# Performance work log

Hardware: AMD Instinct MI355X
Metric: run time of the kernel (lower is better)

The kernel has to match this reference:

```python
import jax, jax.numpy as jnp
import numpy as np

EMBED_DIM = 1024
NUM_HEADS = 16
DEPTH = EMBED_DIM // NUM_HEADS


def setup_inputs() -> dict:
    key = jax.random.key(0)
    ks = jax.random.split(key, 6)
    B, S, D = 2, 2048, EMBED_DIM
    scale = 1.0 / np.sqrt(D)
    return {
        "x": jax.random.normal(ks[0], (B, S, D), dtype=jnp.float32),
        "mask": jax.random.randint(ks[1], (B, S), 0, 2, dtype=jnp.int32),
        "wq_w": jax.random.normal(ks[2], (D, D), dtype=jnp.float32) * scale,
        "wq_b": jnp.zeros((D,), dtype=jnp.float32),
        "wk_w": jax.random.normal(ks[3], (D, D), dtype=jnp.float32) * scale,
        "wk_b": jnp.zeros((D,), dtype=jnp.float32),
        "wv_w": jax.random.normal(ks[4], (D, D), dtype=jnp.float32) * scale,
        "wv_b": jnp.zeros((D,), dtype=jnp.float32),
        "dense_w": jax.random.normal(ks[5], (D, D), dtype=jnp.float32) * scale,
        "dense_b": jnp.zeros((D,), dtype=jnp.float32),
    }


def _split_heads(t, B, S):
    # [B, S, D] -> [B, H, S, depth]
    return t.reshape(B, S, NUM_HEADS, DEPTH).transpose(0, 2, 1, 3)


def reference(x, mask, wq_w, wq_b, wk_w, wk_b, wv_w, wv_b, dense_w, dense_b):
    B, S, D = x.shape
    q = _split_heads(x @ wq_w.T + wq_b, B, S)  # [B, H, S, d]
    k = _split_heads(x @ wk_w.T + wk_b, B, S)
    v = _split_heads(x @ wv_w.T + wv_b, B, S)

    logits = jnp.einsum('bhqd,bhkd->bhqk', q, k) / jnp.sqrt(
        jnp.asarray(DEPTH, dtype=jnp.float32))
    # mask [B, S] broadcast to [B, 1, 1, S] over key axis, additive -1e9
    logits = logits + mask.astype(logits.dtype)[:, None, None, :] * (-1e9)
    attn = jax.nn.softmax(logits, axis=-1)  # [B, H, S, S]
    ctx = jnp.einsum('bhqk,bhkd->bhqd', attn, v)
    ctx = ctx.transpose(0, 2, 1, 3).reshape(B, S, D)
    out = ctx @ dense_w.T + dense_b
    return out, attn
```

## Files before the change

### kernel.cpp

```cpp
#include <hip/hip_runtime.h>


#define S_LEN 2048
#define D_DIM 1024
#define H_NUM 16
#define M_ROWS 4096

typedef __attribute__((ext_vector_type(8))) short bf16x8;
typedef __attribute__((ext_vector_type(4))) float f32x4;

static __device__ __forceinline__ unsigned short f2bf(float f) {
  union { float f; unsigned u; } v; v.f = f;
  unsigned r = (v.u + 0x7FFFu + ((v.u >> 16) & 1u)) >> 16;
  return (unsigned short)r;
}

static __device__ __forceinline__ bf16x8 cvt8(float4 a, float4 b) {
  bf16x8 r;
  r[0] = (short)f2bf(a.x); r[1] = (short)f2bf(a.y);
  r[2] = (short)f2bf(a.z); r[3] = (short)f2bf(a.w);
  r[4] = (short)f2bf(b.x); r[5] = (short)f2bf(b.y);
  r[6] = (short)f2bf(b.z); r[7] = (short)f2bf(b.w);
  return r;
}

template <int AF32, int CF32>
__global__ __launch_bounds__(256) void gemm_bt(
    const void* __restrict__ Ap,
    const float* __restrict__ W0, const float* __restrict__ W1,
    const float* __restrict__ W2,
    const float* __restrict__ b0, const float* __restrict__ b1,
    const float* __restrict__ b2,
    void* __restrict__ C0v, void* __restrict__ C1v, void* __restrict__ C2v,
    int Mdim, int Ndim, int Kdim) {
  const float* W = W0; const float* bias = b0; void* Cv = C0v;
  if (blockIdx.z == 1) { W = W1; bias = b1; Cv = C1v; }
  else if (blockIdx.z == 2) { W = W2; bias = b2; Cv = C2v; }

  __shared__ __align__(16) unsigned short As[128][40];
  __shared__ __align__(16) unsigned short Bs[128][40];

  const int tid = threadIdx.x;
  const int l = tid & 63;
  const int w = tid >> 6;
  const int wm = w >> 1, wn = w & 1;
  const int lo = l & 15, hi = l >> 4;

  const int mBase = blockIdx.y * 128;
  const int nBase = blockIdx.x * 128;

  f32x4 acc[4][4];
  for (int mr = 0; mr < 4; ++mr)
    for (int nr = 0; nr < 4; ++nr) acc[mr][nr] = (f32x4){0.f, 0.f, 0.f, 0.f};

  for (int k0 = 0; k0 < Kdim; k0 += 32) {
    __syncthreads();
    for (int it = 0; it < 2; ++it) {
      int c = tid + it * 256;
      int r = c >> 2, cc = (c & 3) * 8;
      if (AF32) {
        const float* ap = (const float*)Ap + (size_t)(mBase + r) * Kdim + k0 + cc;
        *(bf16x8*)&As[r][cc] = cvt8(((const float4*)ap)[0], ((const float4*)ap)[1]);
      } else {
        *(int4*)&As[r][cc] =
            *(const int4*)((const unsigned short*)Ap + (size_t)(mBase + r) * Kdim + k0 + cc);
      }
      const float* wp = W + (size_t)(nBase + r) * Kdim + k0 + cc;
      *(bf16x8*)&Bs[r][cc] = cvt8(((const float4*)wp)[0], ((const float4*)wp)[1]);
    }
    __syncthreads();
    bf16x8 af[4], bfm[4];
    for (int mr = 0; mr < 4; ++mr)
      af[mr] = *(const bf16x8*)&As[wm * 64 + mr * 16 + lo][hi * 8];
    for (int nr = 0; nr < 4; ++nr)
      bfm[nr] = *(const bf16x8*)&Bs[wn * 64 + nr * 16 + lo][hi * 8];
    for (int mr = 0; mr < 4; ++mr)
      for (int nr = 0; nr < 4; ++nr)
        acc[mr][nr] = __builtin_amdgcn_mfma_f32_16x16x32_bf16(
            af[mr], bfm[nr], acc[mr][nr], 0, 0, 0);
  }

  for (int nr = 0; nr < 4; ++nr) {
    int col = nBase + wn * 64 + nr * 16 + lo;
    float bv = bias[col];
    for (int mr = 0; mr < 4; ++mr) {
      int rbase = mBase + wm * 64 + mr * 16 + hi * 4;
      for (int i = 0; i < 4; ++i) {
        float val = acc[mr][nr][i] + bv;
        if (CF32)
          ((float*)Cv)[(size_t)(rbase + i) * Ndim + col] = val;
        else
          ((unsigned short*)Cv)[(size_t)(rbase + i) * Ndim + col] = f2bf(val);
      }
    }
  }
}

__global__ __launch_bounds__(256) void attn_kernel(
    const unsigned short* __restrict__ qb, const unsigned short* __restrict__ kb,
    const unsigned short* __restrict__ vb, const int* __restrict__ mask,
    float* __restrict__ attn, unsigned short* __restrict__ ctx) {
  const int b = blockIdx.z, h = blockIdx.y, q0 = blockIdx.x * 64;
  const int tid = threadIdx.x, l = tid & 63, w = tid >> 6;
  const int lo = l & 15, hi = l >> 4;

  __shared__ __align__(16) unsigned short k_lds[64][72];
  __shared__ __align__(16) unsigned short vt_lds[64][72];
  __shared__ __align__(16) float p_f32[64][68];

  const size_t qrow = (size_t)(b * S_LEN + q0 + w * 16 + lo) * D_DIM + h * 64;
  bf16x8 qa[2];
  qa[0] = *(const bf16x8*)(qb + qrow + hi * 8);
  qa[1] = *(const bf16x8*)(qb + qrow + 32 + hi * 8);

  const size_t kvbase = (size_t)b * S_LEN * D_DIM + h * 64;
  float rsum[4] = {0.f, 0.f, 0.f, 0.f};

  for (int kt = 0; kt < 32; ++kt) {
    const int key0 = kt * 64;
    __syncthreads();
    for (int it = 0; it < 2; ++it) {
      int c = tid + it * 256;
      int r = c >> 3, cc = (c & 7) * 8;
      *(int4*)&k_lds[r][cc] = *(const int4*)(kb + kvbase + (size_t)(key0 + r) * D_DIM + cc);
    }
    __syncthreads();
    f32x4 acc[4];
    for (int nr = 0; nr < 4; ++nr) acc[nr] = (f32x4){0.f, 0.f, 0.f, 0.f};
    for (int nr = 0; nr < 4; ++nr) {
      bf16x8 kf0 = *(const bf16x8*)&k_lds[nr * 16 + lo][hi * 8];
      bf16x8 kf1 = *(const bf16x8*)&k_lds[nr * 16 + lo][32 + hi * 8];
      acc[nr] = __builtin_amdgcn_mfma_f32_16x16x32_bf16(qa[0], kf0, acc[nr], 0, 0, 0);
      acc[nr] = __builtin_amdgcn_mfma_f32_16x16x32_bf16(qa[1], kf1, acc[nr], 0, 0, 0);
    }
    for (int nr = 0; nr < 4; ++nr) {
      float madd = mask[b * S_LEN + key0 + nr * 16 + lo] ? -1e9f : 0.f;
      for (int i = 0; i < 4; ++i)
        rsum[i] += __expf(acc[nr][i] * 0.125f + madd);
    }
  }
  for (int m = 1; m < 16; m <<= 1)
    for (int i = 0; i < 4; ++i) rsum[i] += __shfl_xor(rsum[i], m);
  float inv[4];
  for (int i = 0; i < 4; ++i) inv[i] = 1.0f / rsum[i];

  f32x4 ctxacc[4];
  for (int nr = 0; nr < 4; ++nr) ctxacc[nr] = (f32x4){0.f, 0.f, 0.f, 0.f};
  const size_t attnbase = (size_t)(b * H_NUM + h) * S_LEN * S_LEN;

  for (int kt = 0; kt < 32; ++kt) {
    const int key0 = kt * 64;
    __syncthreads();
    for (int it = 0; it < 2; ++it) {
      int c = tid + it * 256;
      int r = c >> 3, cc = (c & 7) * 8;
      *(int4*)&k_lds[r][cc] = *(const int4*)(kb + kvbase + (size_t)(key0 + r) * D_DIM + cc);
      bf16x8 vv = *(const bf16x8*)(vb + kvbase + (size_t)(key0 + r) * D_DIM + cc);
      for (int j = 0; j < 8; ++j) vt_lds[cc + j][r] = (unsigned short)vv[j];
    }
    __syncthreads();
    f32x4 acc[4];
    for (int nr = 0; nr < 4; ++nr) acc[nr] = (f32x4){0.f, 0.f, 0.f, 0.f};
    for (int nr = 0; nr < 4; ++nr) {
      bf16x8 kf0 = *(const bf16x8*)&k_lds[nr * 16 + lo][hi * 8];
      bf16x8 kf1 = *(const bf16x8*)&k_lds[nr * 16 + lo][32 + hi * 8];
      acc[nr] = __builtin_amdgcn_mfma_f32_16x16x32_bf16(qa[0], kf0, acc[nr], 0, 0, 0);
      acc[nr] = __builtin_amdgcn_mfma_f32_16x16x32_bf16(qa[1], kf1, acc[nr], 0, 0, 0);
    }
    for (int nr = 0; nr < 4; ++nr) {
      float madd = mask[b * S_LEN + key0 + nr * 16 + lo] ? -1e9f : 0.f;
      for (int i = 0; i < 4; ++i) {
        float p = __expf(acc[nr][i] * 0.125f + madd) * inv[i];
        p_f32[w * 16 + hi * 4 + i][nr * 16 + lo] = p;
      }
    }
    __syncthreads();
    bf16x8 pa0, pa1;
    for (int j = 0; j < 8; ++j) {
      pa0[j] = (short)f2bf(p_f32[w * 16 + lo][hi * 8 + j]);
      pa1[j] = (short)f2bf(p_f32[w * 16 + lo][32 + hi * 8 + j]);
    }
    for (int nr = 0; nr < 4; ++nr) {
      bf16x8 vf0 = *(const bf16x8*)&vt_lds[nr * 16 + lo][hi * 8];
      bf16x8 vf1 = *(const bf16x8*)&vt_lds[nr * 16 + lo][32 + hi * 8];
      ctxacc[nr] = __builtin_amdgcn_mfma_f32_16x16x32_bf16(pa0, vf0, ctxacc[nr], 0, 0, 0);
      ctxacc[nr] = __builtin_amdgcn_mfma_f32_16x16x32_bf16(pa1, vf1, ctxacc[nr], 0, 0, 0);
    }
    for (int it = 0; it < 4; ++it) {
      int c = tid + it * 256;
      int r = c >> 4, cc = (c & 15) * 4;
      *(float4*)(attn + attnbase + (size_t)(q0 + r) * S_LEN + key0 + cc) =
          *(const float4*)&p_f32[r][cc];
    }
  }

  for (int nr = 0; nr < 4; ++nr) {
    int col = h * 64 + nr * 16 + lo;
    for (int i = 0; i < 4; ++i) {
      int row = q0 + w * 16 + hi * 4 + i;
      ctx[(size_t)(b * S_LEN + row) * D_DIM + col] = f2bf(ctxacc[nr][i]);
    }
  }
}

extern "C" void kernel_launch(void* const* d_in, const int* in_sizes, int n_in,
                              void* d_out, int out_size, void* d_ws, size_t ws_size,
                              hipStream_t stream) {
  const float* x    = (const float*)d_in[0];
  const int*   mask = (const int*)d_in[1];
  const float* wq   = (const float*)d_in[2];
  const float* bq   = (const float*)d_in[3];
  const float* wk   = (const float*)d_in[4];
  const float* bk   = (const float*)d_in[5];
  const float* wv   = (const float*)d_in[6];
  const float* bv   = (const float*)d_in[7];
  const float* wd   = (const float*)d_in[8];
  const float* bd   = (const float*)d_in[9];

  float* out  = (float*)d_out;
  float* attn = out + (size_t)M_ROWS * D_DIM;

  unsigned short* ws   = (unsigned short*)d_ws;
  unsigned short* qb   = ws;
  unsigned short* kbuf = ws + 4194304;
  unsigned short* vbuf = ws + 8388608;
  unsigned short* ctxb = ws + 12582912;

  gemm_bt<1, 0><<<dim3(8, 32, 3), 256, 0, stream>>>(
      x, wq, wk, wv, bq, bk, bv, qb, kbuf, vbuf, M_ROWS, D_DIM, D_DIM);

  attn_kernel<<<dim3(32, 16, 2), 256, 0, stream>>>(qb, kbuf, vbuf, mask, attn, ctxb);

  gemm_bt<0, 1><<<dim3(8, 32, 1), 256, 0, stream>>>(
      ctxb, wd, wd, wd, bd, bd, bd, out, out, out, M_ROWS, D_DIM, D_DIM);
}
```

Baseline: 322.6 us.

## Pre-cast QKV inputs to bf16, use direct LDS loads, double attention query tile

Adds separate cast kernels that convert x and the Q/K/V weights to bf16, staging them in the not-yet-written attn output buffer. A new QKV GEMM then loads tiles with global_load_lds over a 64-wide K step instead of converting fp32 on the fly. The attention kernel now covers 128 query rows per block, so each wave computes two 16-row MMA tiles and each K/V tile loaded into LDS is reused twice. It also caches the mask as additive floats in shared memory and vectorises the P-to-bf16 conversion. The costs are extra launches and traffic for the casts, higher LDS use in attention (a larger P buffer plus the mask array), and half as many attention blocks.

```diff
diff --git a/kernel.cpp b/kernel.cpp
--- a/kernel.cpp
+++ b/kernel.cpp
@@ -24,21 +24,39 @@
   return r;
 }
 
-template <int AF32, int CF32>
-__global__ __launch_bounds__(256) void gemm_bt(
-    const void* __restrict__ Ap,
-    const float* __restrict__ W0, const float* __restrict__ W1,
-    const float* __restrict__ W2,
+static __device__ __forceinline__ void gld16(const void* g, void* s) {
+  __builtin_amdgcn_global_load_lds(
+      (const __attribute__((address_space(1))) unsigned int*)g,
+      (__attribute__((address_space(3))) unsigned int*)s, 16, 0, 0);
+}
+
+__global__ __launch_bounds__(256) void cast_f32_bf16(
+    const float* __restrict__ src, unsigned short* __restrict__ dst, int n4) {
+  int i = blockIdx.x * 256 + threadIdx.x;
+  if (i >= n4) return;
+  float4 v = ((const float4*)src)[i];
+  unsigned long long o =
+      (unsigned long long)f2bf(v.x) |
+      ((unsigned long long)f2bf(v.y) << 16) |
+      ((unsigned long long)f2bf(v.z) << 32) |
+      ((unsigned long long)f2bf(v.w) << 48);
+  ((unsigned long long*)dst)[i] = o;
+}
+
+__global__ __launch_bounds__(256) void gemm_qkv(
+    const unsigned short* __restrict__ A,
+    const unsigned short* __restrict__ W0, const unsigned short* __restrict__ W1,
+    const unsigned short* __restrict__ W2,
     const float* __restrict__ b0, const float* __restrict__ b1,
     const float* __restrict__ b2,
-    void* __restrict__ C0v, void* __restrict__ C1v, void* __restrict__ C2v,
-    int Mdim, int Ndim, int Kdim) {
-  const float* W = W0; const float* bias = b0; void* Cv = C0v;
-  if (blockIdx.z == 1) { W = W1; bias = b1; Cv = C1v; }
-  else if (blockIdx.z == 2) { W = W2; bias = b2; Cv = C2v; }
-
-  __shared__ __align__(16) unsigned short As[128][40];
-  __shared__ __align__(16) unsigned short Bs[128][40];
+    unsigned short* __restrict__ C0, unsigned short* __restrict__ C1,
+    unsigned short* __restrict__ C2) {
+  const unsigned short* W = W0; const float* bias = b0; unsigned short* C = C0;
+  if (blockIdx.z == 1) { W = W1; bias = b1; C = C1; }
+  else if (blockIdx.z == 2) { W = W2; bias = b2; C = C2; }
+
+  __shared__ __align__(16) unsigned short As[128 * 64];
+  __shared__ __align__(16) unsigned short Bs[128 * 64];
 
   const int tid = threadIdx.x;
   const int l = tid & 63;
@@ -53,19 +71,65 @@
   for (int mr = 0; mr < 4; ++mr)
     for (int nr = 0; nr < 4; ++nr) acc[mr][nr] = (f32x4){0.f, 0.f, 0.f, 0.f};
 
-  for (int k0 = 0; k0 < Kdim; k0 += 32) {
+  for (int k0 = 0; k0 < 1024; k0 += 64) {
+    __syncthreads();
+    for (int i = 0; i < 4; ++i) {
+      int s = w * 4 + i;
+      int row = s * 8 + (l >> 3), colb = (l & 7) * 8;
+      gld16(A + (size_t)(mBase + row) * 1024 + k0 + colb, As + s * 512);
+      gld16(W + (size_t)(nBase + row) * 1024 + k0 + colb, Bs + s * 512);
+    }
+    __syncthreads();
+    for (int kk = 0; kk < 2; ++kk) {
+      bf16x8 af[4], bfm[4];
+      for (int mr = 0; mr < 4; ++mr)
+        af[mr] = *(const bf16x8*)&As[(wm * 64 + mr * 16 + lo) * 64 + kk * 32 + hi * 8];
+      for (int nr = 0; nr < 4; ++nr)
+        bfm[nr] = *(const bf16x8*)&Bs[(wn * 64 + nr * 16 + lo) * 64 + kk * 32 + hi * 8];
+      for (int mr = 0; mr < 4; ++mr)
+        for (int nr = 0; nr < 4; ++nr)
+          acc[mr][nr] = __builtin_amdgcn_mfma_f32_16x16x32_bf16(
+              af[mr], bfm[nr], acc[mr][nr], 0, 0, 0);
+    }
+  }
+
+  for (int nr = 0; nr < 4; ++nr) {
+    int col = nBase + wn * 64 + nr * 16 + lo;
+    float bv = bias[col];
+    for (int mr = 0; mr < 4; ++mr) {
+      int rbase = mBase + wm * 64 + mr * 16 + hi * 4;
+      for (int i = 0; i < 4; ++i)
+        C[(size_t)(rbase + i) * 1024 + col] = f2bf(acc[mr][nr][i] + bv);
+    }
+  }
+}
+
+__global__ __launch_bounds__(256) void gemm_proj(
+    const unsigned short* __restrict__ A, const float* __restrict__ W,
+    const float* __restrict__ bias, float* __restrict__ C) {
+  __shared__ __align__(16) unsigned short As[128][40];
+  __shared__ __align__(16) unsigned short Bs[128][40];
+
+  const int tid = threadIdx.x;
+  const int l = tid & 63;
+  const int w = tid >> 6;
+  const int wm = w >> 1, wn = w & 1;
+  const int lo = l & 15, hi = l >> 4;
+
+  const int mBase = blockIdx.y * 128;
+  const int nBase = blockIdx.x * 128;
+
+  f32x4 acc[4][4];
+  for (int mr = 0; mr < 4; ++mr)
+    for (int nr = 0; nr < 4; ++nr) acc[mr][nr] = (f32x4){0.f, 0.f, 0.f, 0.f};
+
+  for (int k0 = 0; k0 < 1024; k0 += 32) {
     __syncthreads();
     for (int it = 0; it < 2; ++it) {
       int c = tid + it * 256;
       int r = c >> 2, cc = (c & 3) * 8;
-      if (AF32) {
-        const float* ap = (const float*)Ap + (size_t)(mBase + r) * Kdim + k0 + cc;
-        *(bf16x8*)&As[r][cc] = cvt8(((const float4*)ap)[0], ((const float4*)ap)[1]);
-      } else {
-        *(int4*)&As[r][cc] =
-            *(const int4*)((const unsigned short*)Ap + (size_t)(mBase + r) * Kdim + k0 + cc);
-      }
-      const float* wp = W + (size_t)(nBase + r) * Kdim + k0 + cc;
+      *(int4*)&As[r][cc] = *(const int4*)(A + (size_t)(mBase + r) * 1024 + k0 + cc);
+      const float* wp = W + (size_t)(nBase + r) * 1024 + k0 + cc;
       *(bf16x8*)&Bs[r][cc] = cvt8(((const float4*)wp)[0], ((const float4*)wp)[1]);
     }
     __syncthreads();
@@ -85,13 +149,8 @@
     float bv = bias[col];
     for (int mr = 0; mr < 4; ++mr) {
       int rbase = mBase + wm * 64 + mr * 16 + hi * 4;
-      for (int i = 0; i < 4; ++i) {
-        float val = acc[mr][nr][i] + bv;
-        if (CF32)
-          ((float*)Cv)[(size_t)(rbase + i) * Ndim + col] = val;
-        else
-          ((unsigned short*)Cv)[(size_t)(rbase + i) * Ndim + col] = f2bf(val);
-      }
+      for (int i = 0; i < 4; ++i)
+        C[(size_t)(rbase + i) * 1024 + col] = acc[mr][nr][i] + bv;
     }
   }
 }
@@ -100,21 +159,27 @@
     const unsigned short* __restrict__ qb, const unsigned short* __restrict__ kb,
     const unsigned short* __restrict__ vb, const int* __restrict__ mask,
     float* __restrict__ attn, unsigned short* __restrict__ ctx) {
-  const int b = blockIdx.z, h = blockIdx.y, q0 = blockIdx.x * 64;
+  const int b = blockIdx.z, h = blockIdx.y, q0 = blockIdx.x * 128;
   const int tid = threadIdx.x, l = tid & 63, w = tid >> 6;
   const int lo = l & 15, hi = l >> 4;
 
   __shared__ __align__(16) unsigned short k_lds[64][72];
   __shared__ __align__(16) unsigned short vt_lds[64][72];
-  __shared__ __align__(16) float p_f32[64][68];
-
-  const size_t qrow = (size_t)(b * S_LEN + q0 + w * 16 + lo) * D_DIM + h * 64;
-  bf16x8 qa[2];
-  qa[0] = *(const bf16x8*)(qb + qrow + hi * 8);
-  qa[1] = *(const bf16x8*)(qb + qrow + 32 + hi * 8);
+  __shared__ __align__(16) float p_f32[128][68];
+  __shared__ float madd[S_LEN];
+
+  for (int i = tid; i < S_LEN; i += 256)
+    madd[i] = mask[b * S_LEN + i] ? -1e9f : 0.f;
+
+  bf16x8 qa[2][2];
+  for (int mr = 0; mr < 2; ++mr) {
+    const size_t qrow = (size_t)(b * S_LEN + q0 + w * 32 + mr * 16 + lo) * D_DIM + h * 64;
+    qa[mr][0] = *(const bf16x8*)(qb + qrow + hi * 8);
+    qa[mr][1] = *(const bf16x8*)(qb + qrow + 32 + hi * 8);
+  }
 
   const size_t kvbase = (size_t)b * S_LEN * D_DIM + h * 64;
-  float rsum[4] = {0.f, 0.f, 0.f, 0.f};
+  float rsum[2][4] = {{0.f, 0.f, 0.f, 0.f}, {0.f, 0.f, 0.f, 0.f}};
 
   for (int kt = 0; kt < 32; ++kt) {
     const int key0 = kt * 64;
@@ -125,27 +190,33 @@
       *(int4*)&k_lds[r][cc] = *(const int4*)(kb + kvbase + (size_t)(key0 + r) * D_DIM + cc);
     }
     __syncthreads();
-    f32x4 acc[4];
-    for (int nr = 0; nr < 4; ++nr) acc[nr] = (f32x4){0.f, 0.f, 0.f, 0.f};
+    f32x4 acc[2][4];
+    for (int mr = 0; mr < 2; ++mr)
+      for (int nr = 0; nr < 4; ++nr) acc[mr][nr] = (f32x4){0.f, 0.f, 0.f, 0.f};
+    for (int kk = 0; kk < 2; ++kk)
+      for (int nr = 0; nr < 4; ++nr) {
+        bf16x8 kf = *(const bf16x8*)&k_lds[nr * 16 + lo][kk * 32 + hi * 8];
+        for (int mr = 0; mr < 2; ++mr)
+          acc[mr][nr] = __builtin_amdgcn_mfma_f32_16x16x32_bf16(
+              qa[mr][kk], kf, acc[mr][nr], 0, 0, 0);
+      }
     for (int nr = 0; nr < 4; ++nr) {
-      bf16x8 kf0 = *(const bf16x8*)&k_lds[nr * 16 + lo][hi * 8];
-      bf16x8 kf1 = *(const bf16x8*)&k_lds[nr * 16 + lo][32 + hi * 8];
-      acc[nr] = __builtin_amdgcn_mfma_f32_16x16x32_bf16(qa[0], kf0, acc[nr], 0, 0, 0);
-      acc[nr] = __builtin_amdgcn_mfma_f32_16x16x32_bf16(qa[1], kf1, acc[nr], 0, 0, 0);
-    }
-    for (int nr = 0; nr < 4; ++nr) {
-      float madd = mask[b * S_LEN + key0 + nr * 16 + lo] ? -1e9f : 0.f;
-      for (int i = 0; i < 4; ++i)
-        rsum[i] += __expf(acc[nr][i] * 0.125f + madd);
+      float ma = madd[key0 + nr * 16 + lo];
+      for (int mr = 0; mr < 2; ++mr)
+        for (int i = 0; i < 4; ++i)
+          rsum[mr][i] += __expf(acc[mr][nr][i] * 0.125f + ma);
     }
   }
   for (int m = 1; m < 16; m <<= 1)
-    for (int i = 0; i < 4; ++i) rsum[i] += __shfl_xor(rsum[i], m);
-  float inv[4];
-  for (int i = 0; i < 4; ++i) inv[i] = 1.0f / rsum[i];
-
-  f32x4 ctxacc[4];
-  for (int nr = 0; nr < 4; ++nr) ctxacc[nr] = (f32x4){0.f, 0.f, 0.f, 0.f};
+    for (int mr = 0; mr < 2; ++mr)
+      for (int i = 0; i < 4; ++i) rsum[mr][i] += __shfl_xor(rsum[mr][i], m);
+  float inv[2][4];
+  for (int mr = 0; mr < 2; ++mr)
+    for (int i = 0; i < 4; ++i) inv[mr][i] = 1.0f / rsum[mr][i];
+
+  f32x4 ctxacc[2][4];
+  for (int mr = 0; mr < 2; ++mr)
+    for (int nr = 0; nr < 4; ++nr) ctxacc[mr][nr] = (f32x4){0.f, 0.f, 0.f, 0.f};
   const size_t attnbase = (size_t)(b * H_NUM + h) * S_LEN * S_LEN;
 
   for (int kt = 0; kt < 32; ++kt) {
@@ -159,34 +230,39 @@
       for (int j = 0; j < 8; ++j) vt_lds[cc + j][r] = (unsigned short)vv[j];
     }
     __syncthreads();
-    f32x4 acc[4];
-    for (int nr = 0; nr < 4; ++nr) acc[nr] = (f32x4){0.f, 0.f, 0.f, 0.f};
+    f32x4 acc[2][4];
+    for (int mr = 0; mr < 2; ++mr)
+      for (int nr = 0; nr < 4; ++nr) acc[mr][nr] = (f32x4){0.f, 0.f, 0.f, 0.f};
+    for (int kk = 0; kk < 2; ++kk)
+      for (int nr = 0; nr < 4; ++nr) {
+        bf16x8 kf = *(const bf16x8*)&k_lds[nr * 16 + lo][kk * 32 + hi * 8];
+        for (int mr = 0; mr < 2; ++mr)
+          acc[mr][nr] = __builtin_amdgcn_mfma_f32_16x16x32_bf16(
+              qa[mr][kk], kf, acc[mr][nr], 0, 0, 0);
+      }
     for (int nr = 0; nr < 4; ++nr) {
-      bf16x8 kf0 = *(const bf16x8*)&k_lds[nr * 16 + lo][hi * 8];
-      bf16x8 kf1 = *(const bf16x8*)&k_lds[nr * 16 + lo][32 + hi * 8];
-      acc[nr] = __builtin_amdgcn_mfma_f32_16x16x32_bf16(qa[0], kf0, acc[nr], 0, 0, 0);
-      acc[nr] = __builtin_amdgcn_mfma_f32_16x16x32_bf16(qa[1], kf1, acc[nr], 0, 0, 0);
-    }
-    for (int nr = 0; nr < 4; ++nr) {
-      float madd = mask[b * S_LEN + key0 + nr * 16 + lo] ? -1e9f : 0.f;
-      for (int i = 0; i < 4; ++i) {
-        float p = __expf(acc[nr][i] * 0.125f + madd) * inv[i];
-        p_f32[w * 16 + hi * 4 + i][nr * 16 + lo] = p;
-      }
-    }
-    __syncthreads();
-    bf16x8 pa0, pa1;
-    for (int j = 0; j < 8; ++j) {
-      pa0[j] = (short)f2bf(p_f32[w * 16 + lo][hi * 8 + j]);
-      pa1[j] = (short)f2bf(p_f32[w * 16 + lo][32 + hi * 8 + j]);
-    }
-    for (int nr = 0; nr < 4; ++nr) {
-      bf16x8 vf0 = *(const bf16x8*)&vt_lds[nr * 16 + lo][hi * 8];
-      bf16x8 vf1 = *(const bf16x8*)&vt_lds[nr * 16 + lo][32 + hi * 8];
-      ctxacc[nr] = __builtin_amdgcn_mfma_f32_16x16x32_bf16(pa0, vf0, ctxacc[nr], 0, 0, 0);
-      ctxacc[nr] = __builtin_amdgcn_mfma_f32_16x16x32_bf16(pa1, vf1, ctxacc[nr], 0, 0, 0);
-    }
-    for (int it = 0; it < 4; ++it) {
+      float ma = madd[key0 + nr * 16 + lo];
+      for (int mr = 0; mr < 2; ++mr)
+        for (int i = 0; i < 4; ++i) {
+          float p = __expf(acc[mr][nr][i] * 0.125f + ma) * inv[mr][i];
+          p_f32[w * 32 + mr * 16 + hi * 4 + i][nr * 16 + lo] = p;
+        }
+    }
+    __syncthreads();
+    bf16x8 pa[2][2];
+    for (int mr = 0; mr < 2; ++mr)
+      for (int kk = 0; kk < 2; ++kk) {
+        const float* pr = &p_f32[w * 32 + mr * 16 + lo][kk * 32 + hi * 8];
+        pa[mr][kk] = cvt8(*(const float4*)pr, *(const float4*)(pr + 4));
+      }
+    for (int kk = 0; kk < 2; ++kk)
+      for (int nr = 0; nr < 4; ++nr) {
+        bf16x8 vf = *(const bf16x8*)&vt_lds[nr * 16 + lo][kk * 32 + hi * 8];
+        for (int mr = 0; mr < 2; ++mr)
+          ctxacc[mr][nr] = __builtin_amdgcn_mfma_f32_16x16x32_bf16(
+              pa[mr][kk], vf, ctxacc[mr][nr], 0, 0, 0);
+      }
+    for (int it = 0; it < 8; ++it) {
       int c = tid + it * 256;
       int r = c >> 4, cc = (c & 15) * 4;
       *(float4*)(attn + attnbase + (size_t)(q0 + r) * S_LEN + key0 + cc) =
@@ -196,10 +272,11 @@
 
   for (int nr = 0; nr < 4; ++nr) {
     int col = h * 64 + nr * 16 + lo;
-    for (int i = 0; i < 4; ++i) {
-      int row = q0 + w * 16 + hi * 4 + i;
-      ctx[(size_t)(b * S_LEN + row) * D_DIM + col] = f2bf(ctxacc[nr][i]);
-    }
+    for (int mr = 0; mr < 2; ++mr)
+      for (int i = 0; i < 4; ++i) {
+        int row = q0 + w * 32 + mr * 16 + hi * 4 + i;
+        ctx[(size_t)(b * S_LEN + row) * D_DIM + col] = f2bf(ctxacc[mr][nr][i]);
+      }
   }
 }
 
@@ -220,17 +297,26 @@
   float* out  = (float*)d_out;
   float* attn = out + (size_t)M_ROWS * D_DIM;
 
+  unsigned short* xb  = (unsigned short*)attn;
+  unsigned short* wqb = xb + 4194304;
+  unsigned short* wkb = xb + 5242880;
+  unsigned short* wvb = xb + 6291456;
+
   unsigned short* ws   = (unsigned short*)d_ws;
   unsigned short* qb   = ws;
   unsigned short* kbuf = ws + 4194304;
   unsigned short* vbuf = ws + 8388608;
   unsigned short* ctxb = ws + 12582912;
 
-  gemm_bt<1, 0><<<dim3(8, 32, 3), 256, 0, stream>>>(
-      x, wq, wk, wv, bq, bk, bv, qb, kbuf, vbuf, M_ROWS, D_DIM, D_DIM);
-
-  attn_kernel<<<dim3(32, 16, 2), 256, 0, stream>>>(qb, kbuf, vbuf, mask, attn, ctxb);
-
-  gemm_bt<0, 1><<<dim3(8, 32, 1), 256, 0, stream>>>(
-      ctxb, wd, wd, wd, bd, bd, bd, out, out, out, M_ROWS, D_DIM, D_DIM);
-}
+  cast_f32_bf16<<<4096, 256, 0, stream>>>(x,  xb,  1048576);
+  cast_f32_bf16<<<1024, 256, 0, stream>>>(wq, wqb, 262144);
+  cast_f32_bf16<<<1024, 256, 0, stream>>>(wk, wkb, 262144);
+  cast_f32_bf16<<<1024, 256, 0, stream>>>(wv, wvb, 262144);
+
+  gemm_qkv<<<dim3(8, 32, 3), 256, 0, stream>>>(
+      xb, wqb, wkb, wvb, bq, bk, bv, qb, kbuf, vbuf);
+
+  attn_kernel<<<dim3(16, 16, 2), 256, 0, stream>>>(qb, kbuf, vbuf, mask, attn, ctxb);
+
+  gemm_proj<<<dim3(8, 32), 256, 0, stream>>>(ctxb, wd, bd, out);
+}
```

Result: slower. 332.8 us (+3.2%).
